# Kernel optimization log

Measured on AMD Instinct MI355X. Metric: run time of the kernel, lower is better.

Reference implementation:

```python
import jax, jax.numpy as jnp
import numpy as np

B, C, H, W, K = 64, 64, 32, 32, 512  # batch, embedding_dim, latent HxW, num_embeddings
COMMITMENT_COST = 0.25


def setup_inputs() -> dict:
    key = jax.random.key(0)
    k1, k2 = jax.random.split(key)
    inputs = jax.random.normal(k1, (B, C, H, W), dtype=jnp.float32)
    # nn.Embedding weight initialized uniform(-1/K, 1/K)
    weight = jax.random.uniform(k2, (K, C), minval=-1.0 / K, maxval=1.0 / K, dtype=jnp.float32)
    return {"inputs": inputs, "weight": weight}


def reference(inputs, weight):
    # NCHW -> NHWC
    x = jnp.transpose(inputs, (0, 2, 3, 1))  # [B,H,W,C]
    b, h, w, c = x.shape
    flat = x.reshape(-1, c)  # [N, C], N = B*H*W

    distances = (jnp.sum(flat * flat, axis=1, keepdims=True)
                 + jnp.sum(weight * weight, axis=1)[None, :]
                 - 2.0 * flat @ weight.T)

    idx = jnp.argmin(distances, axis=1)  # [N]
    encodings = jax.nn.one_hot(idx, weight.shape[0], dtype=flat.dtype)  # [N, K]

    # gather codebook vectors (same math as encodings @ weight)
    quantized = weight[idx].reshape(x.shape)  # [B,H,W,C]

    e_latent = jnp.mean((jax.lax.stop_gradient(quantized) - x) ** 2, axis=(1, 2, 3))
    q_latent = jnp.mean((quantized - jax.lax.stop_gradient(x)) ** 2, axis=(1, 2, 3))
    loss = q_latent + COMMITMENT_COST * e_latent  # [B]

    # straight-through estimator
    quantized_st = x + jax.lax.stop_gradient(quantized - x)

    avg_probs = jnp.mean(encodings, axis=0)  # [K]
    perplexity = jnp.exp(-jnp.sum(avg_probs * jnp.log(avg_probs + 1e-10)))

    q_out = jnp.transpose(quantized_st, (0, 3, 1, 2))  # back to NCHW
    enc_idx = idx.reshape(b, -1)  # [B, H*W]
    return (q_out, loss, perplexity, encodings, enc_idx, distances)
```

## Files before the change

### kernel.cpp

```cpp
#include <hip/hip_runtime.h>
#include <stdint.h>
#include <math.h>

#pragma clang fp contract(off)

#define B_   64
#define C_   64
#define HW_  1024
#define K_   512
#define N_   65536

#define OUT_Q    0ull
#define OUT_LOSS 4194304ull
#define OUT_PERP 4194368ull
#define OUT_ENC  4194369ull
#define OUT_IDX  37748801ull
#define OUT_DIST 37814337ull

#define WS_WT     0ull
#define WS_WNORM  131072ull
#define WS_HIST   133120ull
#define WS_SUMSQ  135168ull
#define WS_ZERO_BYTES (512*4 + 64*4)

typedef float f32x4 __attribute__((ext_vector_type(4)));

static __device__ __forceinline__ void nt_store4(float* p, float a, float b,
                                                 float c, float d) {
  f32x4 v = {a, b, c, d};
  __builtin_nontemporal_store(v, (f32x4*)p);
}

__global__ __launch_bounds__(256) void vq_prep(const float* __restrict__ w,
                                               float* __restrict__ wt,
                                               float* __restrict__ wnorm) {
  const int t = threadIdx.x;
  const int g = blockIdx.x * 256 + t;
  const int c = g >> 9;
  const int k = g & 511;
  wt[g] = w[k * 64 + c];

  if (blockIdx.x < 16) {
    const int row = g >> 3;
    const int j = g & 7;
    float s = 0.f;
    for (int i = 0; i < 8; ++i) {
      float v = w[row * 64 + 8 * i + j];
      float sq = v * v;
      s = s + sq;
    }
    float o1 = __shfl_xor(s, 1); s = s + o1;
    float o2 = __shfl_xor(s, 2); s = s + o2;
    float o4 = __shfl_xor(s, 4); s = s + o4;
    if (j == 0) wnorm[row] = s;
  }
}

__global__ __launch_bounds__(256, 4) void vq_dist(const float* __restrict__ x,
                                                  const float* __restrict__ wt,
                                                  const float* __restrict__ wnorm,
                                                  float* __restrict__ out,
                                                  int* __restrict__ hist) {
  __shared__ float x_s[64 * 32];
  __shared__ float an_s[32];

  const int t   = threadIdx.x;
  const int blk = blockIdx.x;
  const int n0  = blk * 32;
  const int b   = n0 >> 10;
  const int hw0 = n0 & 1023;
  const int wid = t >> 6;
  const int l   = t & 63;

  {
    const float* xb = x + (size_t)b * 65536 + hw0;
    const int c0 = t >> 3;
    const int m4 = (t & 7) * 4;
#pragma unroll
    for (int i = 0; i < 2; ++i) {
      int c = i * 32 + c0;
      float4 v = *(const float4*)(xb + (size_t)c * 1024 + m4);
      *(float4*)(&x_s[c * 32 + m4]) = v;
    }
  }
  __syncthreads();

  {
    const int r = t >> 3, j = t & 7;
    float s = 0.f;
#pragma unroll
    for (int i = 0; i < 8; ++i) {
      float v = x_s[(8 * i + j) * 32 + r];
      float sq = v * v;
      s = s + sq;
    }
    float o1 = __shfl_xor(s, 1); s = s + o1;
    float o2 = __shfl_xor(s, 2); s = s + o2;
    float o4 = __shfl_xor(s, 4); s = s + o4;
    if (j == 0) an_s[r] = s;
  }

  float wn[8];
  *(float4*)(wn)     = *(const float4*)(wnorm + 4 * l);
  *(float4*)(wn + 4) = *(const float4*)(wnorm + 256 + 4 * l);

  float acc[8][8];
#pragma unroll
  for (int i = 0; i < 8; ++i)
#pragma unroll
    for (int j = 0; j < 8; ++j) acc[i][j] = 0.f;

  const float* const wl = wt + 4 * l;
  const float* const xw = x_s + 8 * wid;
  float4 w0 = *(const float4*)(wl);
  float4 w1 = *(const float4*)(wl + 256);
#pragma unroll 2
  for (int c = 0; c < 64; ++c) {
    const int cn = (c + 1) & 63;
    const float4 nw0 = *(const float4*)(wl + cn * 512);
    const float4 nw1 = *(const float4*)(wl + cn * 512 + 256);
    float xv[8];
    *(float4*)(xv)     = *(const float4*)(xw + c * 32);
    *(float4*)(xv + 4) = *(const float4*)(xw + c * 32 + 4);
    const float wv0[4] = {w0.x, w0.y, w0.z, w0.w};
    const float wv1[4] = {w1.x, w1.y, w1.z, w1.w};
#pragma unroll
    for (int i = 0; i < 8; ++i) {
#pragma unroll
      for (int j = 0; j < 4; ++j) {
        acc[i][j]     = __builtin_fmaf(xv[i], wv0[j], acc[i][j]);
        acc[i][j + 4] = __builtin_fmaf(xv[i], wv1[j], acc[i][j + 4]);
      }
    }
    w0 = nw0; w1 = nw1;
  }

  const int m_base = 8 * wid;
  float vb[8]; int kb[8];
#pragma unroll
  for (int i = 0; i < 8; ++i) {
    const float an = an_s[m_base + i];
#pragma unroll
    for (int j = 0; j < 8; ++j) {
      float tt = an + wn[j];
      acc[i][j] = __builtin_fmaf(-2.f, acc[i][j], tt);
    }
    float v = acc[i][0]; int k = 4 * l;
#pragma unroll
    for (int j = 1; j < 8; ++j) {
      const int kj = ((j >> 2) << 8) + 4 * l + (j & 3);
      if (acc[i][j] < v) { v = acc[i][j]; k = kj; }
    }
    vb[i] = v; kb[i] = k;
  }

#pragma unroll
  for (int d = 1; d < 64; d <<= 1) {
#pragma unroll
    for (int i = 0; i < 8; ++i) {
      float v2 = __shfl_xor(vb[i], d);
      int   k2 = __shfl_xor(kb[i], d);
      if (v2 < vb[i] || (v2 == vb[i] && k2 < kb[i])) { vb[i] = v2; kb[i] = k2; }
    }
  }

  float* const dist_o = out + OUT_DIST;
#pragma unroll
  for (int i = 0; i < 8; ++i) {
    const int m = m_base + i;
    const size_t n = (size_t)(n0 + m);
    float* dr = dist_o + n * 512;
    nt_store4(dr + 4 * l,       acc[i][0], acc[i][1], acc[i][2], acc[i][3]);
    nt_store4(dr + 256 + 4 * l, acc[i][4], acc[i][5], acc[i][6], acc[i][7]);
    if (l == i) {
      out[OUT_IDX + n] = (float)kb[i];
      atomicAdd(&hist[kb[i]], 1);
    }
  }
}

__global__ __launch_bounds__(256, 8) void vq_q(const float* __restrict__ x,
                                               const float* __restrict__ wt,
                                               float* __restrict__ out,
                                               float* __restrict__ sumsq) {
  __shared__ float red_s[4];

  const int t   = threadIdx.x;
  const int blk = blockIdx.x;
  const int n0  = blk * 32;
  const int b   = n0 >> 10;
  const int hw0 = n0 & 1023;
  const int wid = t >> 6;
  const int l   = t & 63;

  const float* const idx_f = out + OUT_IDX + n0;

  float* const enc_o = out + OUT_ENC;
  const int k0 = 4 * l;
#pragma unroll
  for (int i = 0; i < 8; ++i) {
    const int m = 8 * wid + i;
    const int kbi = (int)idx_f[m];
    float* er = enc_o + (size_t)(n0 + m) * 512;
    nt_store4(er + k0,
              (k0 + 0 == kbi) ? 1.f : 0.f, (k0 + 1 == kbi) ? 1.f : 0.f,
              (k0 + 2 == kbi) ? 1.f : 0.f, (k0 + 3 == kbi) ? 1.f : 0.f);
    nt_store4(er + 256 + k0,
              (k0 + 256 == kbi) ? 1.f : 0.f, (k0 + 257 == kbi) ? 1.f : 0.f,
              (k0 + 258 == kbi) ? 1.f : 0.f, (k0 + 259 == kbi) ? 1.f : 0.f);
  }

  float lsum = 0.f;
  float* const q_o = out + OUT_Q;
#pragma unroll
  for (int it = 0; it < 2; ++it) {
    const int c  = it * 32 + (t >> 3);
    const int m4 = (t & 7) * 4;
    float xq[4];
    *(float4*)(xq) = *(const float4*)(x + (size_t)b * 65536 +
                                      (size_t)c * 1024 + hw0 + m4);
    float qv[4];
#pragma unroll
    for (int u = 0; u < 4; ++u) {
      const int kbm = (int)idx_f[m4 + u];
      qv[u] = wt[(size_t)c * 512 + kbm];
      const float d = qv[u] - xq[u];
      lsum = __builtin_fmaf(d, d, lsum);
    }
    nt_store4(&q_o[(size_t)b * 65536 + (size_t)c * 1024 + hw0 + m4],
              qv[0], qv[1], qv[2], qv[3]);
  }
#pragma unroll
  for (int d = 1; d < 64; d <<= 1) lsum += __shfl_xor(lsum, d);
  if (l == 0) red_s[wid] = lsum;
  __syncthreads();
  if (t == 0) {
    float s = (red_s[0] + red_s[1]) + (red_s[2] + red_s[3]);
    atomicAdd(sumsq + b, s);
  }
}

__global__ __launch_bounds__(512) void vq_fin(const int* __restrict__ hist,
                                              const float* __restrict__ sumsq,
                                              float* __restrict__ out) {
  __shared__ double red[8];
  const int t = threadIdx.x;
  double p = (double)hist[t] * (1.0 / 65536.0);
  double term = p * log(p + 1e-10);
  for (int d = 1; d < 64; d <<= 1) term += __shfl_xor(term, d);
  if ((t & 63) == 0) red[t >> 6] = term;
  __syncthreads();
  if (t == 0) {
    double s = 0.0;
    for (int i = 0; i < 8; ++i) s += red[i];
    out[OUT_PERP] = (float)exp(-s);
  }
  if (t < 64) {
    float m = sumsq[t] * (1.0f / 65536.0f);
    out[OUT_LOSS + t] = m + 0.25f * m;
  }
}

extern "C" void kernel_launch(void* const* d_in, const int* in_sizes, int n_in,
                              void* d_out, int out_size, void* d_ws, size_t ws_size,
                              hipStream_t stream) {
  const float* x = (const float*)d_in[0];
  const float* w = (const float*)d_in[1];
  float* out = (float*)d_out;
  char* ws = (char*)d_ws;
  float* wt    = (float*)(ws + WS_WT);
  float* wnorm = (float*)(ws + WS_WNORM);
  int*   hist  = (int*)  (ws + WS_HIST);
  float* sumsq = (float*)(ws + WS_SUMSQ);

  (void)hipMemsetAsync(ws + WS_HIST, 0, WS_ZERO_BYTES, stream);
  vq_prep<<<128, 256, 0, stream>>>(w, wt, wnorm);
  vq_dist<<<2048, 256, 0, stream>>>(x, wt, wnorm, out, hist);
  vq_q<<<2048, 256, 0, stream>>>(x, wt, out, sumsq);
  vq_fin<<<1, 512, 0, stream>>>(hist, sumsq, out);
}
```

Before: 358.9 us.

## Split distance GEMM into two codebook halves with deeper weight prefetch

The distance kernel now computes the 512 codebook columns in two passes of 256, holding an 8x4 accumulator instead of 8x8, and writes each half's distances and running argmin immediately after it is computed. The weight loads are prefetched four channels ahead instead of one. The aim is to cut register pressure and give more memory-level parallelism, at the cost of streaming the shared x tile twice and rereading the weight matrix for each half. Tie-breaking still favours the lower index because of the strict less-than comparison and the half ordering.

```diff
diff --git a/kernel.cpp b/kernel.cpp
--- a/kernel.cpp
+++ b/kernel.cpp
@@ -100,58 +100,74 @@
     if (j == 0) an_s[r] = s;
   }
 
-  float wn[8];
-  *(float4*)(wn)     = *(const float4*)(wnorm + 4 * l);
-  *(float4*)(wn + 4) = *(const float4*)(wnorm + 256 + 4 * l);
-
-  float acc[8][8];
-#pragma unroll
-  for (int i = 0; i < 8; ++i)
-#pragma unroll
-    for (int j = 0; j < 8; ++j) acc[i][j] = 0.f;
-
-  const float* const wl = wt + 4 * l;
-  const float* const xw = x_s + 8 * wid;
-  float4 w0 = *(const float4*)(wl);
-  float4 w1 = *(const float4*)(wl + 256);
-#pragma unroll 2
-  for (int c = 0; c < 64; ++c) {
-    const int cn = (c + 1) & 63;
-    const float4 nw0 = *(const float4*)(wl + cn * 512);
-    const float4 nw1 = *(const float4*)(wl + cn * 512 + 256);
-    float xv[8];
-    *(float4*)(xv)     = *(const float4*)(xw + c * 32);
-    *(float4*)(xv + 4) = *(const float4*)(xw + c * 32 + 4);
-    const float wv0[4] = {w0.x, w0.y, w0.z, w0.w};
-    const float wv1[4] = {w1.x, w1.y, w1.z, w1.w};
-#pragma unroll
-    for (int i = 0; i < 8; ++i) {
-#pragma unroll
-      for (int j = 0; j < 4; ++j) {
-        acc[i][j]     = __builtin_fmaf(xv[i], wv0[j], acc[i][j]);
-        acc[i][j + 4] = __builtin_fmaf(xv[i], wv1[j], acc[i][j + 4]);
-      }
-    }
-    w0 = nw0; w1 = nw1;
-  }
-
   const int m_base = 8 * wid;
   float vb[8]; int kb[8];
 #pragma unroll
-  for (int i = 0; i < 8; ++i) {
-    const float an = an_s[m_base + i];
-#pragma unroll
-    for (int j = 0; j < 8; ++j) {
-      float tt = an + wn[j];
-      acc[i][j] = __builtin_fmaf(-2.f, acc[i][j], tt);
-    }
-    float v = acc[i][0]; int k = 4 * l;
-#pragma unroll
-    for (int j = 1; j < 8; ++j) {
-      const int kj = ((j >> 2) << 8) + 4 * l + (j & 3);
-      if (acc[i][j] < v) { v = acc[i][j]; k = kj; }
-    }
-    vb[i] = v; kb[i] = k;
+  for (int i = 0; i < 8; ++i) { vb[i] = __builtin_inff(); kb[i] = 0; }
+
+  float* const dist_o = out + OUT_DIST;
+  const float* const xw = x_s + 8 * wid;
+
+#pragma unroll
+  for (int h = 0; h < 2; ++h) {
+    const float* const wl = wt + h * 256 + 4 * l;
+    float wn[4];
+    *(float4*)(wn) = *(const float4*)(wnorm + h * 256 + 4 * l);
+
+    float acc[8][4];
+#pragma unroll
+    for (int i = 0; i < 8; ++i)
+#pragma unroll
+      for (int j = 0; j < 4; ++j) acc[i][j] = 0.f;
+
+#define WLD(cc) (*(const float4*)(wl + (size_t)(cc) * 512))
+    float4 f0 = WLD(0), f1 = WLD(1), f2 = WLD(2), f3 = WLD(3);
+
+#define DBODY(cc, F) {                                                        \
+    float xv[8];                                                              \
+    *(float4*)(xv)     = *(const float4*)(xw + (cc) * 32);                    \
+    *(float4*)(xv + 4) = *(const float4*)(xw + (cc) * 32 + 4);                \
+    const float wv[4] = {(F).x, (F).y, (F).z, (F).w};                         \
+    _Pragma("unroll")                                                         \
+    for (int i_ = 0; i_ < 8; ++i_) {                                          \
+      _Pragma("unroll")                                                       \
+      for (int j_ = 0; j_ < 4; ++j_)                                          \
+        acc[i_][j_] = __builtin_fmaf(xv[i_], wv[j_], acc[i_][j_]);            \
+    } }
+
+#pragma unroll 1
+    for (int c = 0; c < 64; c += 4) {
+      float4 n0v = WLD((c + 4) & 63);
+      float4 n1v = WLD((c + 5) & 63);
+      float4 n2v = WLD((c + 6) & 63);
+      float4 n3v = WLD((c + 7) & 63);
+      DBODY(c + 0, f0)
+      DBODY(c + 1, f1)
+      DBODY(c + 2, f2)
+      DBODY(c + 3, f3)
+      f0 = n0v; f1 = n1v; f2 = n2v; f3 = n3v;
+    }
+#undef DBODY
+#undef WLD
+
+#pragma unroll
+    for (int i = 0; i < 8; ++i) {
+      const int m = m_base + i;
+      const float an = an_s[m];
+      float D[4];
+#pragma unroll
+      for (int j = 0; j < 4; ++j) {
+        float tt = an + wn[j];
+        D[j] = __builtin_fmaf(-2.f, acc[i][j], tt);
+      }
+#pragma unroll
+      for (int j = 0; j < 4; ++j) {
+        const int kj = h * 256 + 4 * l + j;
+        if (D[j] < vb[i]) { vb[i] = D[j]; kb[i] = kj; }
+      }
+      nt_store4(dist_o + (size_t)(n0 + m) * 512 + h * 256 + 4 * l,
+                D[0], D[1], D[2], D[3]);
+    }
   }
 
 #pragma unroll
@@ -164,15 +180,10 @@
     }
   }
 
-  float* const dist_o = out + OUT_DIST;
 #pragma unroll
   for (int i = 0; i < 8; ++i) {
-    const int m = m_base + i;
-    const size_t n = (size_t)(n0 + m);
-    float* dr = dist_o + n * 512;
-    nt_store4(dr + 4 * l,       acc[i][0], acc[i][1], acc[i][2], acc[i][3]);
-    nt_store4(dr + 256 + 4 * l, acc[i][4], acc[i][5], acc[i][6], acc[i][7]);
     if (l == i) {
+      const size_t n = (size_t)(n0 + m_base + i);
       out[OUT_IDX + n] = (float)kb[i];
       atomicAdd(&hist[kb[i]], 1);
     }
```

Result: slower. 371.2 us (+3.4%).
